# Kernel optimization log

Hardware: AMD Instinct MI355X
Metric: run time of the kernel (lower is better)

Reference implementation:

```python
import jax, jax.numpy as jnp
import numpy as np

DN = ('NCHW', 'OIHW', 'NCHW')
A, NC = 3, 80  # num_anchors, num_classes


def conv(x, w, b, pad=1):
    y = jax.lax.conv_general_dilated(x, w, (1, 1), [(pad, pad), (pad, pad)], dimension_numbers=DN)
    return y + b[None, :, None, None]


def up2(x):
    return jnp.repeat(jnp.repeat(x, 2, axis=2), 2, axis=3)


def gen_anchors():
    # AnchorGenerator: sizes per level, 3 aspect ratios, 1 scale, stride=2**(i+3)
    sizes = [32.0, 64.0, 128.0]
    ars = [0.5, 1.0, 2.0]
    hw = [(64, 64), (32, 32), (16, 16)]
    out = []
    for i, ((h, w), bs) in enumerate(zip(hw, sizes)):
        stride = 2.0 ** (i + 3)
        base = np.array([[-bs * np.sqrt(a) / 2, -bs / np.sqrt(a) / 2,
                          bs * np.sqrt(a) / 2, bs / np.sqrt(a) / 2] for a in ars], dtype=np.float32)
        sx = np.arange(w, dtype=np.float32) * stride
        sy = np.arange(h, dtype=np.float32) * stride
        yy, xx = np.meshgrid(sy, sx, indexing='ij')  # torch.meshgrid default 'ij'
        shifts = np.stack([xx.ravel(), yy.ravel(), xx.ravel(), yy.ravel()], axis=1)
        anc = (base[None, :, :] + shifts[:, None, :]).reshape(-1, 4)
        out.append(anc)
    return jnp.asarray(np.concatenate(out, axis=0))


def setup_inputs() -> dict:
    key = jax.random.key(0)
    ks = jax.random.split(key, 32)
    def w(k, o, i, kh, kw):
        return jax.random.normal(k, (o, i, kh, kw), jnp.float32) * 0.02
    B = 8
    inp = {
        'feat3': jax.random.normal(ks[0], (B, 512, 64, 64), jnp.float32),
        'feat4': jax.random.normal(ks[1], (B, 1024, 32, 32), jnp.float32),
        'feat5': jax.random.normal(ks[2], (B, 2048, 16, 16), jnp.float32),
        # FPN lateral 1x1 convs
        'lw0': w(ks[3], 256, 512, 1, 1),  'lb0': jnp.zeros(256, jnp.float32),
        'lw1': w(ks[4], 256, 1024, 1, 1), 'lb1': jnp.zeros(256, jnp.float32),
        'lw2': w(ks[5], 256, 2048, 1, 1), 'lb2': jnp.zeros(256, jnp.float32),
        # FPN 3x3 output convs
        'fw0': w(ks[6], 256, 256, 3, 3), 'fb0': jnp.zeros(256, jnp.float32),
        'fw1': w(ks[7], 256, 256, 3, 3), 'fb1': jnp.zeros(256, jnp.float32),
        'fw2': w(ks[8], 256, 256, 3, 3), 'fb2': jnp.zeros(256, jnp.float32),
        # cls tower (shared across levels)
        'cw0': w(ks[9], 256, 256, 3, 3),  'cb0': jnp.zeros(256, jnp.float32),
        'cw1': w(ks[10], 256, 256, 3, 3), 'cb1': jnp.zeros(256, jnp.float32),
        'cw2': w(ks[11], A * NC, 256, 3, 3), 'cb2': jnp.zeros(A * NC, jnp.float32),
        # reg tower (shared across levels)
        'rw0': w(ks[12], 256, 256, 3, 3), 'rb0': jnp.zeros(256, jnp.float32),
        'rw1': w(ks[13], 256, 256, 3, 3), 'rb1': jnp.zeros(256, jnp.float32),
        'rw2': w(ks[14], A * 4, 256, 3, 3), 'rb2': jnp.zeros(A * 4, jnp.float32),
    }
    return inp


def _tower(f, w0, b0, w1, b1, w2, b2):
    x = jax.nn.relu(conv(f, w0, b0))
    x = jax.nn.relu(conv(x, w1, b1))
    return conv(x, w2, b2)


def reference(feat3, feat4, feat5,
              lw0, lb0, lw1, lb1, lw2, lb2,
              fw0, fb0, fw1, fb1, fw2, fb2,
              cw0, cb0, cw1, cb1, cw2, cb2,
              rw0, rb0, rw1, rb1, rw2, rb2):
    B = feat3.shape[0]
    # FPN: lateral 1x1 convs + top-down nearest upsample fusion + 3x3 convs
    l0 = conv(feat3, lw0, lb0, pad=0)
    l1 = conv(feat4, lw1, lb1, pad=0)
    l2 = conv(feat5, lw2, lb2, pad=0)
    l1 = l1 + up2(l2)
    l0 = l0 + up2(l1)
    feats = [conv(l0, fw0, fb0), conv(l1, fw1, fb1), conv(l2, fw2, fb2)]
    cls_list, reg_list = [], []
    for f in feats:
        c = _tower(f, cw0, cb0, cw1, cb1, cw2, cb2)  # [B, A*NC, H, W]
        r = _tower(f, rw0, rb0, rw1, rb1, rw2, rb2)  # [B, A*4, H, W]
        H, W = c.shape[2], c.shape[3]
        # view(B, A, C, HW).permute(0, 3, 1, 2) -> [B, HW, A, C]
        c = c.reshape(B, A, NC, H * W).transpose(0, 3, 1, 2)
        r = r.reshape(B, A, 4, H * W).transpose(0, 3, 1, 2)
        cls_list.append(c.reshape(B, H * W, A * NC))
        reg_list.append(r.reshape(B, H * W, A * 4))
    cls_all = jnp.concatenate(cls_list, axis=1)   # [B, 5376, 240]
    reg_all = jnp.concatenate(reg_list, axis=1)   # [B, 5376, 12]
    out = jnp.concatenate([cls_all, reg_all], axis=-1)  # [B, 5376, 252]
    anchors = gen_anchors()  # [16128, 4]
    return out, anchors
```

## Files before the change

kernel.cpp:

```cpp
#include <hip/hip_runtime.h>

typedef __bf16 bf16_t;
typedef __bf16 bf16x8 __attribute__((ext_vector_type(8)));
typedef float f32x4 __attribute__((ext_vector_type(4)));

__device__ inline void gl_lds16(const bf16_t* g, bf16_t* l) {
  __builtin_amdgcn_global_load_lds(
      (const __attribute__((address_space(1))) void*)g,
      (__attribute__((address_space(3))) void*)l, 16, 0, 0);
}

__global__ __launch_bounds__(256)
void nchw_to_nhwc(const float* __restrict__ in, bf16_t* __restrict__ out,
                  int C, int HW) {
  __shared__ float tile[64][65];
  const int n = blockIdx.z;
  const int c0 = blockIdx.y * 64, p0 = blockIdx.x * 64;
  const int t = threadIdx.x;
  const float* src = in + ((size_t)n * C + c0) * HW + p0;
  const int cl = t >> 6;
  const int pl = t & 63;
#pragma unroll
  for (int i = 0; i < 16; ++i)
    tile[cl + i * 4][pl] = src[(size_t)(cl + i * 4) * HW + pl];
  __syncthreads();
  bf16_t* dst = out + ((size_t)n * HW + p0) * C + c0;
  const int pc = t >> 6;
  const int cc = t & 63;
#pragma unroll
  for (int i = 0; i < 16; ++i)
    dst[(size_t)(pc + i * 4) * C + cc] = (bf16_t)tile[cc][pc + i * 4];
}

struct WSrc {
  const float *lw0, *lw1, *lw2;
  const float* w9[9];
  int O9[9];
};
__global__ __launch_bounds__(256)
void weight_prep(WSrc s, bf16_t* __restrict__ LWT0, bf16_t* __restrict__ LWT1,
                 bf16_t* __restrict__ LWT2, bf16_t* __restrict__ W33) {
  int idx = blockIdx.x * 256 + threadIdx.x;
  if (idx < 131072) { LWT0[idx] = (bf16_t)s.lw0[idx]; return; }
  if (idx < 393216) { int i = idx - 131072; LWT1[i] = (bf16_t)s.lw1[i]; return; }
  if (idx < 917504) { int i = idx - 393216; LWT2[i] = (bf16_t)s.lw2[i]; return; }
  int t2 = idx - 917504;
  if (t2 >= 9 * 589824) return;
  int sgi = t2 / 589824;
  int r = t2 - sgi * 589824;
  int kid = r >> 16;
  int rem = r & 65535;
  int o = rem >> 8, ci = rem & 255;
  const float* src = s.w9[sgi];
  int O = s.O9[sgi];
  W33[t2] = (o < O) ? (bf16_t)src[((size_t)o * 256 + ci) * 9 + kid] : (bf16_t)0.0f;
}

__global__ __launch_bounds__(256)
void up2_add_p(bf16_t* __restrict__ dst, const bf16_t* __restrict__ src,
               int lw, int lhw, int dWp, int dNs, int sWp, int sNs, int tot8) {
  int idx = blockIdx.x * 256 + threadIdx.x;
  if (idx >= tot8) return;
  const int c8 = idx & 31;
  const int pos = idx >> 5;
  const int n = pos >> lhw;
  const int rem = pos & ((1 << lhw) - 1);
  const int y = rem >> lw, x = rem & ((1 << lw) - 1);
  bf16_t* d = dst + ((size_t)n * dNs + (y + 1) * dWp + (x + 1)) * 256 + c8 * 8;
  const bf16_t* sp = src + ((size_t)n * sNs + ((y >> 1) + 1) * sWp + ((x >> 1) + 1)) * 256 + c8 * 8;
  bf16x8 dv = *(bf16x8*)d;
  bf16x8 sv = *(const bf16x8*)sp;
#pragma unroll
  for (int k = 0; k < 8; ++k) dv[k] = (bf16_t)((float)dv[k] + (float)sv[k]);
  *(bf16x8*)d = dv;
}

struct Job1 {
  const bf16_t* A;
  const bf16_t* Wt;
  const float* bias;
  bf16_t* outb;
  int mtiles, lw, lhw, oWp, onstride, Cin, pad0, pad1;
};
struct Job1Pack { Job1 j[3]; };

__global__ __launch_bounds__(256, 2)
void conv1_batch(Job1Pack jp) {
  __shared__ __align__(16) bf16_t As[2][128 * 32];
  __shared__ __align__(16) bf16_t Bs[2][128 * 32];
  const int cpx = gridDim.x >> 3;
  int b = (blockIdx.x & 7) * cpx + (blockIdx.x >> 3);
  int ji = 0;
#pragma unroll 1
  for (; ji < 2; ++ji) {
    int sz = jp.j[ji].mtiles * 2;
    if (b < sz) break;
    b -= sz;
  }
  const Job1 J = jp.j[ji];
  const int nt = b & 1, mt = b >> 1;
  const int m0 = mt * 128, n0 = nt * 128;
  const int t = threadIdx.x, l = t & 63, w = t >> 6;
  const int W = 1 << J.lw, HW = 1 << J.lhw;
  const int sr = l >> 2, seg = (l & 3) * 8;
  const bf16_t* aptr[2];
  const bf16_t* bptr[2];
  int lrow[2];
#pragma unroll
  for (int q = 0; q < 2; ++q) {
    const int r = w * 32 + q * 16 + sr;
    aptr[q] = J.A + (size_t)(m0 + r) * J.Cin + seg;
    bptr[q] = J.Wt + (size_t)(n0 + r) * J.Cin + seg;
    lrow[q] = (w * 32 + q * 16) * 32;
  }
  const int fr = l & 15, qd = l >> 4;
  const int wm = (w & 1) * 64, wn = (w >> 1) * 64;

  f32x4 acc[4][4];
#pragma unroll
  for (int i = 0; i < 4; ++i)
#pragma unroll
    for (int j = 0; j < 4; ++j)
#pragma unroll
      for (int r = 0; r < 4; ++r) acc[i][j][r] = 0.0f;

  auto stage = [&](int buf, int kk) {
#pragma unroll
    for (int q = 0; q < 2; ++q) {
      gl_lds16(aptr[q] + (size_t)kk * 32, &As[buf][lrow[q]]);
      gl_lds16(bptr[q] + (size_t)kk * 32, &Bs[buf][lrow[q]]);
    }
  };

  stage(0, 0);

  const int kiters = J.Cin >> 5;
#pragma unroll 1
  for (int kk = 0; kk < kiters; ++kk) {
    const int cur = kk & 1;
    __syncthreads();
    if (kk + 1 < kiters) stage(cur ^ 1, kk + 1);
    bf16x8 af[4], bfv[4];
#pragma unroll
    for (int i = 0; i < 4; ++i)
      af[i] = *(const bf16x8*)&As[cur][(wm + i * 16 + fr) * 32 + qd * 8];
#pragma unroll
    for (int j = 0; j < 4; ++j)
      bfv[j] = *(const bf16x8*)&Bs[cur][(wn + j * 16 + fr) * 32 + qd * 8];
#pragma unroll
    for (int i = 0; i < 4; ++i)
#pragma unroll
      for (int j = 0; j < 4; ++j)
        acc[i][j] = __builtin_amdgcn_mfma_f32_16x16x32_bf16(af[i], bfv[j],
                                                            acc[i][j], 0, 0, 0);
  }

#pragma unroll
  for (int i = 0; i < 4; ++i) {
    const int mrow = m0 + wm + i * 16 + qd * 4;
#pragma unroll
    for (int j = 0; j < 4; ++j) {
      const int co = n0 + wn + j * 16 + fr;
      const float bv = J.bias[co];
#pragma unroll
      for (int r = 0; r < 4; ++r) {
        float v = acc[i][j][r] + bv;
        const int m = mrow + r;
        const int n = m >> J.lhw, hw = m & (HW - 1);
        const int y = hw >> J.lw, x = hw & (W - 1);
        J.outb[((size_t)n * J.onstride + (y + 1) * J.oWp + (x + 1)) * 256 + co] =
            (bf16_t)v;
      }
    }
  }
}

struct Job3 {
  const bf16_t* A;
  const bf16_t* Wt;
  const float* bias;
  bf16_t* outb;
  const bf16_t* Wt2;
  const float* bias2;
  bf16_t* outb2;
  int mtiles, ntiles, lw, lhw, Wp, nsA, oWp, onstride;
  int relu, Cout, pos_off, ch_off, use_outf, nAr, Pc, pad_;
};
struct Job3Pack { Job3 j[6]; };

__global__ __launch_bounds__(256, 3)
void conv3_batch(Job3Pack jp, float* __restrict__ outf) {
  __shared__ __align__(16) bf16_t As[320 * 32];
  __shared__ __align__(16) bf16_t Bs[384 * 32];
  const int cpx = gridDim.x >> 3;
  int b = (blockIdx.x & 7) * cpx + (blockIdx.x >> 3);
  int ji = 0;
#pragma unroll 1
  for (; ji < 5; ++ji) {
    int sz = jp.j[ji].mtiles * jp.j[ji].ntiles;
    if (b < sz) break;
    b -= sz;
  }
  const Job3 J = jp.j[ji];
  int s, mt;
  if (J.ntiles == 4)      { s = b & 3; mt = b >> 2; }
  else if (J.ntiles == 2) { s = b & 1; mt = b >> 1; }
  else                    { s = 0;     mt = b; }
  const int second = (s >= 2);
  const int n0 = (s & 1) * 128;
  const bf16_t* Wtp = second ? J.Wt2 : J.Wt;
  const float* biasp = second ? J.bias2 : J.bias;
  bf16_t* outbp = second ? J.outb2 : J.outb;
  const int m0 = mt * 128;
  const int t = threadIdx.x, l = t & 63, w = t >> 6;
  const int W = 1 << J.lw, HW = 1 << J.lhw;
  const int sr = l >> 2, seg = (l & 3) * 8;
  const int fr = l & 15, qd = l >> 4;
  const int wm = (w & 1) * 64, wn = (w >> 1) * 64;

  const int n_img = m0 >> J.lhw;
  const int Y0 = (m0 & (HW - 1)) >> J.lw;
  const bf16_t* Ag = J.A + ((size_t)n_img * J.nsA + (size_t)Y0 * J.Wp) * 256;

  int apix[4];
#pragma unroll
  for (int i = 0; i < 4; ++i) {
    const int m = wm + i * 16 + fr;
    const int y = m >> J.lw, x = m & (W - 1);
    apix[i] = ((y + 1) * J.Wp + (x + 1)) * 32 + qd * 8;
  }

  f32x4 acc[4][4];
#pragma unroll
  for (int i = 0; i < 4; ++i)
#pragma unroll
    for (int j = 0; j < 4; ++j)
#pragma unroll
      for (int r = 0; r < 4; ++r) acc[i][j][r] = 0.0f;

#pragma unroll 1
  for (int cb = 0; cb < 8; ++cb) {
    const int cboff = cb * 32;
#pragma unroll 1
    for (int ky = 0; ky < 3; ++ky) {
      __syncthreads();
#pragma unroll
      for (int r = 0; r < 6; ++r) {
        const int R = r * 64 + w * 16 + sr;
        const int tp = R >> 7, co = R & 127;
        gl_lds16(Wtp + (size_t)(ky * 3 + tp) * 65536 +
                     (size_t)(n0 + co) * 256 + cboff + seg,
                 &Bs[(r * 64 + w * 16) * 32]);
      }
      if (ky == 0) {
#pragma unroll 1
        for (int r = 0; r < J.nAr; ++r) {
          int p = r * 64 + w * 16 + sr;
          p = (p < J.Pc) ? p : (J.Pc - 1);
          gl_lds16(Ag + (size_t)p * 256 + cboff + seg,
                   &As[(r * 64 + w * 16) * 32]);
        }
      }
      __syncthreads();
      const int dyoff = (ky - 1) * J.Wp * 32;
#pragma unroll
      for (int kx = 0; kx < 3; ++kx) {
        const int d = dyoff + (kx - 1) * 32;
        bf16x8 af[4], bfv[4];
#pragma unroll
        for (int i = 0; i < 4; ++i)
          af[i] = *(const bf16x8*)&As[apix[i] + d];
#pragma unroll
        for (int j = 0; j < 4; ++j)
          bfv[j] = *(const bf16x8*)&Bs[(kx * 128 + wn + j * 16 + fr) * 32 + qd * 8];
#pragma unroll
        for (int i = 0; i < 4; ++i)
#pragma unroll
          for (int j = 0; j < 4; ++j)
            acc[i][j] = __builtin_amdgcn_mfma_f32_16x16x32_bf16(af[i], bfv[j],
                                                                acc[i][j], 0, 0, 0);
      }
    }
  }

#pragma unroll
  for (int i = 0; i < 4; ++i) {
    const int mrow = m0 + wm + i * 16 + qd * 4;
#pragma unroll
    for (int j = 0; j < 4; ++j) {
      const int co = n0 + wn + j * 16 + fr;
      if (co < J.Cout) {
        const float bv = biasp[co];
#pragma unroll
        for (int r = 0; r < 4; ++r) {
          float v = acc[i][j][r] + bv;
          if (J.relu) v = fmaxf(v, 0.0f);
          const int m = mrow + r;
          const int n = m >> J.lhw, hw = m & (HW - 1);
          if (J.use_outf) {
            outf[((size_t)n * 5376 + J.pos_off + hw) * 252 + J.ch_off + co] = v;
          } else {
            const int y = hw >> J.lw, x = hw & (W - 1);
            outbp[((size_t)n * J.onstride + (y + 1) * J.oWp + (x + 1)) * 256 + co] =
                (bf16_t)v;
          }
        }
      }
    }
  }
}

__global__ __launch_bounds__(256)
void anchors_k(float* __restrict__ out) {
  int r = blockIdx.x * 256 + threadIdx.x;
  if (r >= 16128) return;
  int local, w, stride;
  float bs;
  if (r < 12288)      { local = r;          w = 64; stride = 8;  bs = 32.f;  }
  else if (r < 15360) { local = r - 12288;  w = 32; stride = 16; bs = 64.f;  }
  else                { local = r - 15360;  w = 16; stride = 32; bs = 128.f; }
  const int a = local % 3;
  const int s = local / 3;
  const int y = s / w, x = s - y * w;
  const float ar = (a == 0) ? 0.5f : (a == 1) ? 1.0f : 2.0f;
  const float sq = sqrtf(ar);
  const float hw_ = bs * sq * 0.5f, hh = bs / sq * 0.5f;
  const float cx = (float)x * (float)stride, cy = (float)y * (float)stride;
  out[(size_t)r * 4 + 0] = cx - hw_;
  out[(size_t)r * 4 + 1] = cy - hh;
  out[(size_t)r * 4 + 2] = cx + hw_;
  out[(size_t)r * 4 + 3] = cy + hh;
}

extern "C" void kernel_launch(void* const* d_in, const int* in_sizes, int n_in,
                              void* d_out, int out_size, void* d_ws, size_t ws_size,
                              hipStream_t stream) {
  const float* feat3 = (const float*)d_in[0];
  const float* feat4 = (const float*)d_in[1];
  const float* feat5 = (const float*)d_in[2];
  const float* lw0 = (const float*)d_in[3];  const float* lb0 = (const float*)d_in[4];
  const float* lw1 = (const float*)d_in[5];  const float* lb1 = (const float*)d_in[6];
  const float* lw2 = (const float*)d_in[7];  const float* lb2 = (const float*)d_in[8];
  const float* fw0 = (const float*)d_in[9];  const float* fb0 = (const float*)d_in[10];
  const float* fw1 = (const float*)d_in[11]; const float* fb1 = (const float*)d_in[12];
  const float* fw2 = (const float*)d_in[13]; const float* fb2 = (const float*)d_in[14];
  const float* cw0 = (const float*)d_in[15]; const float* cb0 = (const float*)d_in[16];
  const float* cw1 = (const float*)d_in[17]; const float* cb1 = (const float*)d_in[18];
  const float* cw2 = (const float*)d_in[19]; const float* cb2 = (const float*)d_in[20];
  const float* rw0 = (const float*)d_in[21]; const float* rb0 = (const float*)d_in[22];
  const float* rw1 = (const float*)d_in[23]; const float* rb1 = (const float*)d_in[24];
  const float* rw2 = (const float*)d_in[25]; const float* rb2 = (const float*)d_in[26];

  char* ws = (char*)d_ws;
  float* out = (float*)d_out;

  bf16_t* XS3 = (bf16_t*)(ws + 0);
  bf16_t* XS4 = (bf16_t*)(ws + 33554432);
  bf16_t* XS5 = (bf16_t*)(ws + 50331648);
  bf16_t* Lp0 = (bf16_t*)(ws + 58720256);
  bf16_t* Lp1 = (bf16_t*)(ws + 76562432);
  bf16_t* Lp2 = (bf16_t*)(ws + 81297408);
  bf16_t* Pp0 = (bf16_t*)(ws + 82624512);
  bf16_t* Pp1 = (bf16_t*)(ws + 100466688);
  bf16_t* Pp2 = (bf16_t*)(ws + 105201664);
  bf16_t* LWT0 = (bf16_t*)(ws + 106528768);
  bf16_t* LWT1 = (bf16_t*)(ws + 106790912);
  bf16_t* LWT2 = (bf16_t*)(ws + 107315200);
  bf16_t* W33  = (bf16_t*)(ws + 108363776);
  bf16_t* FWT0 = W33 + 0 * 589824;
  bf16_t* FWT1 = W33 + 1 * 589824;
  bf16_t* FWT2 = W33 + 2 * 589824;
  bf16_t* CWT0 = W33 + 3 * 589824;
  bf16_t* CWT1 = W33 + 4 * 589824;
  bf16_t* CWT2 = W33 + 5 * 589824;
  bf16_t* RWT0 = W33 + 6 * 589824;
  bf16_t* RWT1 = W33 + 7 * 589824;
  bf16_t* RWT2 = W33 + 8 * 589824;
  bf16_t* TAc0 = (bf16_t*)(ws + 0);
  bf16_t* TAr0 = (bf16_t*)(ws + 17842176);
  bf16_t* TAc1 = (bf16_t*)(ws + 35684352);
  bf16_t* TAr1 = (bf16_t*)(ws + 40419328);
  bf16_t* TAc2 = (bf16_t*)(ws + 45154304);
  bf16_t* TAr2 = (bf16_t*)(ws + 46481408);
  bf16_t* TBc0 = Pp0; bf16_t* TBr0 = Lp0;
  bf16_t* TBc1 = Pp1; bf16_t* TBr1 = Lp1;
  bf16_t* TBc2 = Pp2; bf16_t* TBr2 = Lp2;

  WSrc wsrc;
  wsrc.lw0 = lw0; wsrc.lw1 = lw1; wsrc.lw2 = lw2;
  const float* w9s[9] = {fw0, fw1, fw2, cw0, cw1, cw2, rw0, rw1, rw2};
  int o9s[9] = {256, 256, 256, 256, 256, 240, 256, 256, 12};
  for (int i = 0; i < 9; ++i) { wsrc.w9[i] = w9s[i]; wsrc.O9[i] = o9s[i]; }
  weight_prep<<<dim3(24320), 256, 0, stream>>>(wsrc, LWT0, LWT1, LWT2, W33);

  nchw_to_nhwc<<<dim3(64, 8, 8),  256, 0, stream>>>(feat3, XS3, 512, 4096);
  nchw_to_nhwc<<<dim3(16, 16, 8), 256, 0, stream>>>(feat4, XS4, 1024, 1024);
  nchw_to_nhwc<<<dim3(4, 32, 8),  256, 0, stream>>>(feat5, XS5, 2048, 256);

  hipMemsetAsync(ws + 58720256, 0, 47808512, stream);

  {
    Job1Pack jp;
    jp.j[0] = {XS3, LWT0, lb0, Lp0, 256, 6, 12, 66, 4356, 512, 0, 0};
    jp.j[1] = {XS4, LWT1, lb1, Lp1, 64, 5, 10, 34, 1156, 1024, 0, 0};
    jp.j[2] = {XS5, LWT2, lb2, Lp2, 16, 4, 8, 18, 324, 2048, 0, 0};
    conv1_batch<<<dim3(672), 256, 0, stream>>>(jp);
  }

  hipMemsetAsync(ws + 0, 0, 47808512, stream);

  up2_add_p<<<dim3(1024), 256, 0, stream>>>(Lp1, Lp2, 5, 10, 34, 1156, 18, 324, 262144);
  up2_add_p<<<dim3(4096), 256, 0, stream>>>(Lp0, Lp1, 6, 12, 66, 4356, 34, 1156, 1048576);

  auto mk3 = [](const bf16_t* A, const bf16_t* Wt, const float* bias,
                bf16_t* outb, int mtiles, int ntiles, int lw, int lhw,
                int Wp, int nsA, int oWp, int onstride, int relu, int Cout,
                int pos_off, int ch_off, int use_outf, int nAr, int Pc) {
    Job3 j;
    j.A = A; j.Wt = Wt; j.bias = bias; j.outb = outb;
    j.Wt2 = Wt; j.bias2 = bias; j.outb2 = outb;
    j.mtiles = mtiles; j.ntiles = ntiles; j.lw = lw; j.lhw = lhw;
    j.Wp = Wp; j.nsA = nsA; j.oWp = oWp; j.onstride = onstride;
    j.relu = relu; j.Cout = Cout; j.pos_off = pos_off; j.ch_off = ch_off;
    j.use_outf = use_outf; j.nAr = nAr; j.Pc = Pc; j.pad_ = 0;
    return j;
  };

  {
    Job3Pack jp;
    jp.j[0] = mk3(Lp0, FWT0, fb0, Pp0, 256, 2, 6, 12, 66, 4356, 66, 4356, 0, 256, 0, 0, 0, 5, 264);
    jp.j[1] = mk3(Lp1, FWT1, fb1, Pp1, 64, 2, 5, 10, 34, 1156, 34, 1156, 0, 256, 0, 0, 0, 4, 204);
    jp.j[2] = mk3(Lp2, FWT2, fb2, Pp2, 16, 2, 4, 8, 18, 324, 18, 324, 0, 256, 0, 0, 0, 3, 180);
    jp.j[3] = jp.j[4] = jp.j[5] = jp.j[2];
    jp.j[3].mtiles = jp.j[4].mtiles = jp.j[5].mtiles = 0;
    conv3_batch<<<dim3(672), 256, 0, stream>>>(jp, out);
  }

  {
    Job3Pack jp;
    jp.j[0] = mk3(Pp0, CWT0, cb0, TAc0, 256, 4, 6, 12, 66, 4356, 66, 4356, 1, 256, 0, 0, 0, 5, 264);
    jp.j[0].Wt2 = RWT0; jp.j[0].bias2 = rb0; jp.j[0].outb2 = TAr0;
    jp.j[1] = mk3(Pp1, CWT0, cb0, TAc1, 64, 4, 5, 10, 34, 1156, 34, 1156, 1, 256, 0, 0, 0, 4, 204);
    jp.j[1].Wt2 = RWT0; jp.j[1].bias2 = rb0; jp.j[1].outb2 = TAr1;
    jp.j[2] = mk3(Pp2, CWT0, cb0, TAc2, 16, 4, 4, 8, 18, 324, 18, 324, 1, 256, 0, 0, 0, 3, 180);
    jp.j[2].Wt2 = RWT0; jp.j[2].bias2 = rb0; jp.j[2].outb2 = TAr2;
    jp.j[3] = jp.j[4] = jp.j[5] = jp.j[2];
    jp.j[3].mtiles = jp.j[4].mtiles = jp.j[5].mtiles = 0;
    conv3_batch<<<dim3(1344), 256, 0, stream>>>(jp, out);
  }

  {
    Job3Pack jp;
    jp.j[0] = mk3(TAc0, CWT1, cb1, TBc0, 256, 2, 6, 12, 66, 4356, 66, 4356, 1, 256, 0, 0, 0, 5, 264);
    jp.j[1] = mk3(TAr0, RWT1, rb1, TBr0, 256, 2, 6, 12, 66, 4356, 66, 4356, 1, 256, 0, 0, 0, 5, 264);
    jp.j[2] = mk3(TAc1, CWT1, cb1, TBc1, 64, 2, 5, 10, 34, 1156, 34, 1156, 1, 256, 0, 0, 0, 4, 204);
    jp.j[3] = mk3(TAr1, RWT1, rb1, TBr1, 64, 2, 5, 10, 34, 1156, 34, 1156, 1, 256, 0, 0, 0, 4, 204);
    jp.j[4] = mk3(TAc2, CWT1, cb1, TBc2, 16, 2, 4, 8, 18, 324, 18, 324, 1, 256, 0, 0, 0, 3, 180);
    jp.j[5] = mk3(TAr2, RWT1, rb1, TBr2, 16, 2, 4, 8, 18, 324, 18, 324, 1, 256, 0, 0, 0, 3, 180);
    conv3_batch<<<dim3(1344), 256, 0, stream>>>(jp, out);
  }

  {
    Job3Pack jp;
    jp.j[0] = mk3(TBc0, CWT2, cb2, nullptr, 256, 2, 6, 12, 66, 4356, 0, 0, 0, 240, 0, 0, 1, 5, 264);
    jp.j[1] = mk3(TBr0, RWT2, rb2, nullptr, 256, 1, 6, 12, 66, 4356, 0, 0, 0, 12, 0, 240, 1, 5, 264);
    jp.j[2] = mk3(TBc1, CWT2, cb2, nullptr, 64, 2, 5, 10, 34, 1156, 0, 0, 0, 240, 4096, 0, 1, 4, 204);
    jp.j[3] = mk3(TBr1, RWT2, rb2, nullptr, 64, 1, 5, 10, 34, 1156, 0, 0, 0, 12, 4096, 240, 1, 4, 204);
    jp.j[4] = mk3(TBc2, CWT2, cb2, nullptr, 16, 2, 4, 8, 18, 324, 0, 0, 0, 240, 5120, 0, 1, 3, 180);
    jp.j[5] = mk3(TBr2, RWT2, rb2, nullptr, 16, 1, 4, 8, 18, 324, 0, 0, 0, 12, 5120, 240, 1, 3, 180);
    conv3_batch<<<dim3(1008), 256, 0, stream>>>(jp, out);
  }

  anchors_k<<<dim3(63), 256, 0, stream>>>(out + 10838016);
}
```

Before: 674.1 us.

## Triple-buffer weight staging with counted vmcnt waits in conv kernels

Moves the 1x1 conv GEMM from a double-buffered to a triple-buffered LDS pipeline, prefetching two K-steps ahead. Barriers become explicit s_waitcnt vmcnt(N) plus s_barrier, so loads still in flight do not stall the current step. In the 3x3 conv, weights are staged per tap in three 128-row buffers instead of all three taps of a row at once, which overlaps global-to-LDS weight loads with MFMA work. The next channel block's activations are loaded after an extra barrier. The cost is more LDS in conv1, a more fragile hand-counted wait scheme, and a serial point at each channel-block boundary where activations are reloaded.

```diff
diff --git a/kernel.cpp b/kernel.cpp
--- a/kernel.cpp
+++ b/kernel.cpp
@@ -86,8 +86,8 @@
 
 __global__ __launch_bounds__(256, 2)
 void conv1_batch(Job1Pack jp) {
-  __shared__ __align__(16) bf16_t As[2][128 * 32];
-  __shared__ __align__(16) bf16_t Bs[2][128 * 32];
+  __shared__ __align__(16) bf16_t As[3][128 * 32];
+  __shared__ __align__(16) bf16_t Bs[3][128 * 32];
   const int cpx = gridDim.x >> 3;
   int b = (blockIdx.x & 7) * cpx + (blockIdx.x >> 3);
   int ji = 0;
@@ -133,13 +133,23 @@
   };
 
   stage(0, 0);
+  stage(1, 1);
 
   const int kiters = J.Cin >> 5;
+  int cur = 0;
 #pragma unroll 1
   for (int kk = 0; kk < kiters; ++kk) {
-    const int cur = kk & 1;
-    __syncthreads();
-    if (kk + 1 < kiters) stage(cur ^ 1, kk + 1);
+    __builtin_amdgcn_sched_barrier(0);
+    if (kk == kiters - 1)
+      asm volatile("s_waitcnt vmcnt(0)\ns_barrier" ::: "memory");
+    else
+      asm volatile("s_waitcnt vmcnt(4)\ns_barrier" ::: "memory");
+    __builtin_amdgcn_sched_barrier(0);
+    if (kk + 2 < kiters) {
+      int nb = cur + 2; if (nb >= 3) nb -= 3;
+      stage(nb, kk + 2);
+    }
+    __builtin_amdgcn_sched_barrier(0);
     bf16x8 af[4], bfv[4];
 #pragma unroll
     for (int i = 0; i < 4; ++i)
@@ -153,6 +163,7 @@
       for (int j = 0; j < 4; ++j)
         acc[i][j] = __builtin_amdgcn_mfma_f32_16x16x32_bf16(af[i], bfv[j],
                                                             acc[i][j], 0, 0, 0);
+    cur = (cur == 2) ? 0 : cur + 1;
   }
 
 #pragma unroll
@@ -191,7 +202,7 @@
 __global__ __launch_bounds__(256, 3)
 void conv3_batch(Job3Pack jp, float* __restrict__ outf) {
   __shared__ __align__(16) bf16_t As[320 * 32];
-  __shared__ __align__(16) bf16_t Bs[384 * 32];
+  __shared__ __align__(16) bf16_t Bs[3][128 * 32];
   const int cpx = gridDim.x >> 3;
   int b = (blockIdx.x & 7) * cpx + (blockIdx.x >> 3);
   int ji = 0;
@@ -238,33 +249,51 @@
 #pragma unroll
       for (int r = 0; r < 4; ++r) acc[i][j][r] = 0.0f;
 
+  const bf16_t* Bgl = Wtp + (size_t)(n0 + w * 16 + sr) * 256 + seg;
+  auto stageB = [&](int buf, int tap, int cboff) {
+    const bf16_t* src = Bgl + (size_t)tap * 65536 + cboff;
+    gl_lds16(src, &Bs[buf][(w * 16) * 32]);
+    gl_lds16(src + 64 * 256, &Bs[buf][(64 + w * 16) * 32]);
+  };
+  auto stageA = [&](int cboff) {
+#pragma unroll 1
+    for (int r = 0; r < J.nAr; ++r) {
+      int p = r * 64 + w * 16 + sr;
+      p = (p < J.Pc) ? p : (J.Pc - 1);
+      gl_lds16(Ag + (size_t)p * 256 + cboff + seg,
+               &As[(r * 64 + w * 16) * 32]);
+    }
+  };
+
+  stageA(0);
+  stageB(0, 0, 0);
+  stageB(1, 1, 0);
+
+  int cur = 0;
 #pragma unroll 1
   for (int cb = 0; cb < 8; ++cb) {
-    const int cboff = cb * 32;
 #pragma unroll 1
     for (int ky = 0; ky < 3; ++ky) {
-      __syncthreads();
-#pragma unroll
-      for (int r = 0; r < 6; ++r) {
-        const int R = r * 64 + w * 16 + sr;
-        const int tp = R >> 7, co = R & 127;
-        gl_lds16(Wtp + (size_t)(ky * 3 + tp) * 65536 +
-                     (size_t)(n0 + co) * 256 + cboff + seg,
-                 &Bs[(r * 64 + w * 16) * 32]);
-      }
-      if (ky == 0) {
-#pragma unroll 1
-        for (int r = 0; r < J.nAr; ++r) {
-          int p = r * 64 + w * 16 + sr;
-          p = (p < J.Pc) ? p : (J.Pc - 1);
-          gl_lds16(Ag + (size_t)p * 256 + cboff + seg,
-                   &As[(r * 64 + w * 16) * 32]);
+      const int dyoff = (ky - 1) * J.Wp * 32;
+#pragma unroll
+      for (int kx = 0; kx < 3; ++kx) {
+        const int tp = ky * 3 + kx;
+        __builtin_amdgcn_sched_barrier(0);
+        if ((tp == 0 && cb > 0) || (tp == 8 && cb == 7)) {
+          asm volatile("s_waitcnt vmcnt(0)\ns_barrier" ::: "memory");
+        } else {
+          asm volatile("s_waitcnt vmcnt(2)\ns_barrier" ::: "memory");
         }
-      }
-      __syncthreads();
-      const int dyoff = (ky - 1) * J.Wp * 32;
-#pragma unroll
-      for (int kx = 0; kx < 3; ++kx) {
+        __builtin_amdgcn_sched_barrier(0);
+        {
+          int t2 = tp + 2, cb2 = cb;
+          if (t2 >= 9) { t2 -= 9; cb2 += 1; }
+          if (cb2 < 8) {
+            int nb = cur + 2; if (nb >= 3) nb -= 3;
+            stageB(nb, t2, cb2 * 32);
+          }
+        }
+        __builtin_amdgcn_sched_barrier(0);
         const int d = dyoff + (kx - 1) * 32;
         bf16x8 af[4], bfv[4];
 #pragma unroll
@@ -272,13 +301,20 @@
           af[i] = *(const bf16x8*)&As[apix[i] + d];
 #pragma unroll
         for (int j = 0; j < 4; ++j)
-          bfv[j] = *(const bf16x8*)&Bs[(kx * 128 + wn + j * 16 + fr) * 32 + qd * 8];
+          bfv[j] = *(const bf16x8*)&Bs[cur][(wn + j * 16 + fr) * 32 + qd * 8];
 #pragma unroll
         for (int i = 0; i < 4; ++i)
 #pragma unroll
           for (int j = 0; j < 4; ++j)
             acc[i][j] = __builtin_amdgcn_mfma_f32_16x16x32_bf16(af[i], bfv[j],
                                                                 acc[i][j], 0, 0, 0);
+        if (tp == 8 && cb < 7) {
+          __builtin_amdgcn_sched_barrier(0);
+          __builtin_amdgcn_s_barrier();
+          __builtin_amdgcn_sched_barrier(0);
+          stageA((cb + 1) * 32);
+        }
+        cur = (cur == 2) ? 0 : cur + 1;
       }
     }
   }
```

After: 706.9 us. 1.05x slower.
